# Kernel tuning notes

Measured on AMD Instinct MI355X. Metric: run time of the kernel, lower is better.

## Reference

```python
import jax, jax.numpy as jnp
import numpy as np

B = 131072
HIDDEN = [512, 512, 512, 512]
BETA = 20.0  # Softplus(beta=20)


def setup_inputs() -> dict:
    key = jax.random.key(0)
    dims = [3] + HIDDEN + [2]  # in_dim=3, out = div_mat_dim + 1 = 2
    n_layers = len(dims) - 1
    ks = jax.random.split(key, 1 + 2 * n_layers)
    d = {"tx": jax.random.normal(ks[0], (B, 3), dtype=jnp.float32)}
    for i, (din, dout) in enumerate(zip(dims[:-1], dims[1:])):
        lim = 1.0 / np.sqrt(din)  # torch nn.Linear default init
        d[f"W{i}"] = jax.random.uniform(ks[1 + 2 * i], (dout, din), jnp.float32, -lim, lim)
        d[f"b{i}"] = jax.random.uniform(ks[2 + 2 * i], (dout,), jnp.float32, -lim, lim)
    return d


def reference(tx, W0, b0, W1, b1, W2, b2, W3, b3, W4, b4):
    params = [(W0, b0), (W1, b1), (W2, b2), (W3, b3), (W4, b4)]

    def mlp(x):
        h = x
        for W, b in params[:-1]:
            # torch Softplus(beta=20): softplus(beta*x)/beta
            h = jax.nn.softplus(BETA * (h @ W.T + b)) / BETA
        W, b = params[-1]
        return h @ W.T + b  # [..., 2]: (stream fn s, pressure p)

    # div_A_matrix builds the 2x2 antisymmetric matrix A with A[0,1]=s, A[1,0]=-s.
    # vmap(jacrev(div_A_matrix)) then einsum('...ii') over the spatial cols (x,y)
    # reduces exactly to u = (ds/dy, -ds/dx). Per-sample grads of s are obtained
    # with one vectorized backward pass (samples are independent).
    g = jax.grad(lambda t: mlp(t)[:, 0].sum())(tx)  # [B, 3] cols = (t, x, y)
    u = jnp.stack([g[:, 2], -g[:, 1]], axis=1)      # [B, 2]
    p = mlp(tx)[:, -1:]                              # [B, 1]
    # torch .squeeze(0) is a no-op for B > 1
    return jnp.concatenate([u, p], axis=1)           # [B, 3]
```

## Files before the change

kernel.cpp:

```cpp
#include <hip/hip_runtime.h>

typedef _Float16 f16;
typedef __attribute__((ext_vector_type(8))) _Float16 f16x8;
typedef __attribute__((ext_vector_type(4))) float f32x4;

#define BT   131072
#define DD   512
#define TM   32
#define MEFF 96
#define NBLK (BT / TM)

__device__ __forceinline__ void stA(char* ab, int row, int colbyte, float v) {
    *(f16*)(ab + row * 1024 + (colbyte ^ ((row & 7) << 4))) = (f16)v;
}
__device__ __forceinline__ f16x8 ldA8(const char* ab, int row, int kbyte) {
    return *(const f16x8*)(ab + row * 1024 + (kbyte ^ ((row & 7) << 4)));
}

__device__ __forceinline__ f16x8 cvt8(const float* q) {
    float4 u0 = *(const float4*)q;
    float4 u1 = *(const float4*)(q + 4);
    f16x8 r;
    r[0] = (f16)u0.x; r[1] = (f16)u0.y; r[2] = (f16)u0.z; r[3] = (f16)u0.w;
    r[4] = (f16)u1.x; r[5] = (f16)u1.y; r[6] = (f16)u1.z; r[7] = (f16)u1.w;
    return r;
}

__global__ void prep_w(const float* __restrict__ W1, const float* __restrict__ W2,
                       const float* __restrict__ W3, f16* __restrict__ wp) {
    int tid = blockIdx.x * 256 + threadIdx.x;
    if (tid >= 3 * 16 * 32 * 64) return;
    int lane = tid & 63;
    int frag = tid >> 6;
    int nsub = frag & 31;
    int sk   = (frag >> 5) & 15;
    int l    = frag >> 9;
    const float* W = (l == 0) ? W1 : (l == 1) ? W2 : W3;
    int n = nsub * 16 + (lane & 15);
    int k = sk * 32 + (lane >> 4) * 8;
    ((f16x8*)wp)[tid] = cvt8(W + n * DD + k);
}

#define MFMA_SK(skc, Q0, Q1, Q2, Q3)                                           \
    _Pragma("unroll")                                                          \
    for (int m = 0; m < 6; ++m) {                                              \
        f16x8 a = ldA8(ab, m * 16 + l15, (skc) * 64 + g16 * 16);               \
        acc[m][0] = __builtin_amdgcn_mfma_f32_16x16x32_f16(a, Q0, acc[m][0], 0, 0, 0); \
        acc[m][1] = __builtin_amdgcn_mfma_f32_16x16x32_f16(a, Q1, acc[m][1], 0, 0, 0); \
        acc[m][2] = __builtin_amdgcn_mfma_f32_16x16x32_f16(a, Q2, acc[m][2], 0, 0, 0); \
        acc[m][3] = __builtin_amdgcn_mfma_f32_16x16x32_f16(a, Q3, acc[m][3], 0, 0, 0); \
    }

#define LOADB(Q0, Q1, Q2, Q3, skc)                                             \
    if constexpr (PREP) {                                                      \
        const f16x8* p = wB + (size_t)((skc) * 32) * 64;                       \
        Q0 = p[0]; Q1 = p[64]; Q2 = p[128]; Q3 = p[192];                       \
    } else {                                                                   \
        const float* q = Wl + (size_t)(wv * 64 + l15) * DD + (skc) * 32 + g16 * 8; \
        Q0 = cvt8(q);                                                          \
        Q1 = cvt8(q + 16 * DD);                                                \
        Q2 = cvt8(q + 32 * DD);                                                \
        Q3 = cvt8(q + 48 * DD);                                                \
    }

template<bool PREP>
__global__ __launch_bounds__(512) void mlp_fused(
    const float* __restrict__ tx,
    const float* __restrict__ W0, const float* __restrict__ b0v,
    const float* __restrict__ W1, const float* __restrict__ b1v,
    const float* __restrict__ W2, const float* __restrict__ b2v,
    const float* __restrict__ W3, const float* __restrict__ b3v,
    const float* __restrict__ W4, const float* __restrict__ b4v,
    const f16* __restrict__ wp, float* __restrict__ out)
{
    __shared__ __align__(16) short abuf_s[MEFF * DD];
    __shared__ float txb[TM * 3];
    char* ab = (char*)abuf_s;

    const int tid  = threadIdx.x;
    const int lane = tid & 63;
    const int wv   = tid >> 6;
    const int g16  = lane >> 4;
    const int l15  = lane & 15;
    const long s0  = (long)blockIdx.x * TM;

    if (tid < TM * 3) txb[tid] = tx[s0 * 3 + tid];
    __syncthreads();

    {
        int n = tid;
        float w0 = W0[n * 3 + 0], w1 = W0[n * 3 + 1], w2 = W0[n * 3 + 2], bb = b0v[n];
        #pragma unroll 4
        for (int s = 0; s < TM; ++s) {
            float z  = fmaf(w0, txb[s * 3], fmaf(w1, txb[s * 3 + 1], fmaf(w2, txb[s * 3 + 2], bb)));
            float aa = fabsf(z);
            float e  = __expf(-20.f * aa);
            float dd = 1.f + e;
            float h  = fmaxf(z, 0.f) + __logf(dd) * 0.05f;
            float sg = (z > 0.f ? 1.f : e) * __builtin_amdgcn_rcpf(dd);
            stA(ab, s,          n * 2, h);
            stA(ab, TM + s,     n * 2, sg * w1);
            stA(ab, 2 * TM + s, n * 2, sg * w2);
        }
    }
    __syncthreads();

    for (int l = 0; l < 3; ++l) {
        const float* Wl = (l == 0) ? W1 : (l == 1) ? W2 : W3;
        const float* bl = (l == 0) ? b1v : (l == 1) ? b2v : b3v;
        const f16x8* wB = (const f16x8*)wp + (size_t)l * (16 * 32 * 64)
                        + (size_t)(wv * 4) * 64 + lane;

        f32x4 acc[6][4];
        #pragma unroll
        for (int m = 0; m < 6; ++m)
            #pragma unroll
            for (int n = 0; n < 4; ++n)
                acc[m][n] = f32x4{0.f, 0.f, 0.f, 0.f};

        f16x8 B0, B1, B2, B3, C0, C1, C2, C3;
        LOADB(B0, B1, B2, B3, 0)
        #pragma unroll 2
        for (int sk = 0; sk < 16; sk += 2) {
            LOADB(C0, C1, C2, C3, sk + 1)
            MFMA_SK(sk, B0, B1, B2, B3)
            if (sk + 2 < 16) { LOADB(B0, B1, B2, B3, sk + 2) }
            MFMA_SK(sk + 1, C0, C1, C2, C3)
        }

        __syncthreads();

        #pragma unroll
        for (int m = 0; m < 2; ++m)
            #pragma unroll
            for (int n = 0; n < 4; ++n) {
                float bias = bl[wv * 64 + n * 16 + l15];
                int   cb   = (wv * 64 + n * 16 + l15) * 2;
                #pragma unroll
                for (int r = 0; r < 4; ++r) {
                    int row = m * 16 + g16 * 4 + r;
                    float z  = acc[m][n][r] + bias;
                    float aa = fabsf(z);
                    float e  = __expf(-20.f * aa);
                    float dd = 1.f + e;
                    float h  = fmaxf(z, 0.f) + __logf(dd) * 0.05f;
                    float sg = (z > 0.f ? 1.f : e) * __builtin_amdgcn_rcpf(dd);
                    stA(ab, row,      cb, h);
                    stA(ab, row + 32, cb, sg * acc[m + 2][n][r]);
                    stA(ab, row + 64, cb, sg * acc[m + 4][n][r]);
                }
            }
        __syncthreads();
    }

    {
        const int kb = lane * 8;
        float wsr[8], wpr[8];
        #pragma unroll
        for (int j = 0; j < 8; ++j) { wsr[j] = W4[kb + j]; wpr[j] = W4[DD + kb + j]; }
        float bp = b4v[1];
        #pragma unroll
        for (int i = 0; i < 4; ++i) {
            int s = wv * 4 + i;
            f16x8 hh = ldA8(ab, s,      lane * 16);
            f16x8 hx = ldA8(ab, 32 + s, lane * 16);
            f16x8 hy = ldA8(ab, 64 + s, lane * 16);
            float dy = 0.f, dx = 0.f, dp = 0.f;
            #pragma unroll
            for (int j = 0; j < 8; ++j) {
                dy = fmaf(wsr[j], (float)hy[j], dy);
                dx = fmaf(wsr[j], (float)hx[j], dx);
                dp = fmaf(wpr[j], (float)hh[j], dp);
            }
            #pragma unroll
            for (int mk = 1; mk < 64; mk <<= 1) {
                dy += __shfl_xor(dy, mk);
                dx += __shfl_xor(dx, mk);
                dp += __shfl_xor(dp, mk);
            }
            if (lane == 0) {
                float* o = out + (s0 + s) * 3;
                o[0] = dy;
                o[1] = -dx;
                o[2] = dp + bp;
            }
        }
    }
}

extern "C" void kernel_launch(void* const* d_in, const int* in_sizes, int n_in,
                              void* d_out, int out_size, void* d_ws, size_t ws_size,
                              hipStream_t stream) {
    const float* tx = (const float*)d_in[0];
    const float* W0 = (const float*)d_in[1]; const float* b0 = (const float*)d_in[2];
    const float* W1 = (const float*)d_in[3]; const float* b1 = (const float*)d_in[4];
    const float* W2 = (const float*)d_in[5]; const float* b2 = (const float*)d_in[6];
    const float* W3 = (const float*)d_in[7]; const float* b3 = (const float*)d_in[8];
    const float* W4 = (const float*)d_in[9]; const float* b4 = (const float*)d_in[10];
    float* out = (float*)d_out;

    const size_t need = (size_t)3 * 512 * 512 * sizeof(f16);
    if (ws_size >= need) {
        f16* wp = (f16*)d_ws;
        prep_w<<<(3 * 16 * 32 * 64 + 255) / 256, 256, 0, stream>>>(W1, W2, W3, wp);
        mlp_fused<true><<<NBLK, 512, 0, stream>>>(tx, W0, b0, W1, b1, W2, b2, W3, b3, W4, b4, wp, out);
    } else {
        mlp_fused<false><<<NBLK, 512, 0, stream>>>(tx, W0, b0, W1, b1, W2, b2, W3, b3, W4, b4, nullptr, out);
    }
}
```

Baseline: 758.8 us.

## Replace block barriers with per-chunk LDS flags so waves start on ready K-chunks

Replaces the __syncthreads barriers between layers with LDS flag counters. Each wave publishes readiness of the two K-chunks (64 columns) it writes, and starts its GEMM loop at its own chunk, rotating through the rest, so it can begin on freshly written data while other waves finish their epilogues. A progress counter stands in for the barrier that guards overwriting the activation buffer. This adds spin-wait overhead and loses the double-buffered B-fragment prefetch, since loads now sit right before each wait, and it relies on workgroup-scope atomics ordering the LDS stores.

```diff
diff --git a/kernel.cpp b/kernel.cpp
--- a/kernel.cpp
+++ b/kernel.cpp
@@ -24,6 +24,15 @@
     r[0] = (f16)u0.x; r[1] = (f16)u0.y; r[2] = (f16)u0.z; r[3] = (f16)u0.w;
     r[4] = (f16)u1.x; r[5] = (f16)u1.y; r[6] = (f16)u1.z; r[7] = (f16)u1.w;
     return r;
+}
+
+__device__ __forceinline__ void waitge(int* p, int v) {
+    if (__hip_atomic_load(p, __ATOMIC_ACQUIRE, __HIP_MEMORY_SCOPE_WORKGROUP) >= v) return;
+    while (__hip_atomic_load(p, __ATOMIC_ACQUIRE, __HIP_MEMORY_SCOPE_WORKGROUP) < v)
+        __builtin_amdgcn_s_sleep(1);
+}
+__device__ __forceinline__ void st_rel(int* p, int v) {
+    __hip_atomic_store(p, v, __ATOMIC_RELEASE, __HIP_MEMORY_SCOPE_WORKGROUP);
 }
 
 __global__ void prep_w(const float* __restrict__ W1, const float* __restrict__ W2,
@@ -41,22 +50,22 @@
     ((f16x8*)wp)[tid] = cvt8(W + n * DD + k);
 }
 
-#define MFMA_SK(skc, Q0, Q1, Q2, Q3)                                           \
+#define MFMA_SK(cc, Q0, Q1, Q2, Q3)                                            \
     _Pragma("unroll")                                                          \
     for (int m = 0; m < 6; ++m) {                                              \
-        f16x8 a = ldA8(ab, m * 16 + l15, (skc) * 64 + g16 * 16);               \
+        f16x8 a = ldA8(ab, m * 16 + l15, (cc) * 64 + g16 * 16);                \
         acc[m][0] = __builtin_amdgcn_mfma_f32_16x16x32_f16(a, Q0, acc[m][0], 0, 0, 0); \
         acc[m][1] = __builtin_amdgcn_mfma_f32_16x16x32_f16(a, Q1, acc[m][1], 0, 0, 0); \
         acc[m][2] = __builtin_amdgcn_mfma_f32_16x16x32_f16(a, Q2, acc[m][2], 0, 0, 0); \
         acc[m][3] = __builtin_amdgcn_mfma_f32_16x16x32_f16(a, Q3, acc[m][3], 0, 0, 0); \
     }
 
-#define LOADB(Q0, Q1, Q2, Q3, skc)                                             \
+#define LOADB(Q0, Q1, Q2, Q3, cc)                                              \
     if constexpr (PREP) {                                                      \
-        const f16x8* p = wB + (size_t)((skc) * 32) * 64;                       \
+        const f16x8* p = wB + ((size_t)(cc) << 11);                            \
         Q0 = p[0]; Q1 = p[64]; Q2 = p[128]; Q3 = p[192];                       \
     } else {                                                                   \
-        const float* q = Wl + (size_t)(wv * 64 + l15) * DD + (skc) * 32 + g16 * 8; \
+        const float* q = Wl + (size_t)(wv * 64 + l15) * DD + (cc) * 32 + g16 * 8; \
         Q0 = cvt8(q);                                                          \
         Q1 = cvt8(q + 16 * DD);                                                \
         Q2 = cvt8(q + 32 * DD);                                                \
@@ -75,6 +84,8 @@
 {
     __shared__ __align__(16) short abuf_s[MEFF * DD];
     __shared__ float txb[TM * 3];
+    __shared__ int ready[16];
+    __shared__ int progress[8];
     char* ab = (char*)abuf_s;
 
     const int tid  = threadIdx.x;
@@ -84,6 +95,8 @@
     const int l15  = lane & 15;
     const long s0  = (long)blockIdx.x * TM;
 
+    if (tid < 16) ready[tid] = 0;
+    if (tid >= 16 && tid < 24) progress[tid - 16] = 0;
     if (tid < TM * 3) txb[tid] = tx[s0 * 3 + tid];
     __syncthreads();
 
@@ -103,12 +116,12 @@
             stA(ab, 2 * TM + s, n * 2, sg * w2);
         }
     }
-    __syncthreads();
-
-    for (int l = 0; l < 3; ++l) {
-        const float* Wl = (l == 0) ? W1 : (l == 1) ? W2 : W3;
-        const float* bl = (l == 0) ? b1v : (l == 1) ? b2v : b3v;
-        const f16x8* wB = (const f16x8*)wp + (size_t)l * (16 * 32 * 64)
+    if (lane == 0) { st_rel(&ready[2 * wv], 1); st_rel(&ready[2 * wv + 1], 1); }
+
+    for (int li = 0; li < 3; ++li) {
+        const float* Wl = (li == 0) ? W1 : (li == 1) ? W2 : W3;
+        const float* bl = (li == 0) ? b1v : (li == 1) ? b2v : b3v;
+        const f16x8* wB = (const f16x8*)wp + (size_t)li * (16 * 32 * 64)
                         + (size_t)(wv * 4) * 64 + lane;
 
         f32x4 acc[6][4];
@@ -118,17 +131,19 @@
             for (int n = 0; n < 4; ++n)
                 acc[m][n] = f32x4{0.f, 0.f, 0.f, 0.f};
 
-        f16x8 B0, B1, B2, B3, C0, C1, C2, C3;
-        LOADB(B0, B1, B2, B3, 0)
+        int c = 2 * wv;
         #pragma unroll 2
-        for (int sk = 0; sk < 16; sk += 2) {
-            LOADB(C0, C1, C2, C3, sk + 1)
-            MFMA_SK(sk, B0, B1, B2, B3)
-            if (sk + 2 < 16) { LOADB(B0, B1, B2, B3, sk + 2) }
-            MFMA_SK(sk + 1, C0, C1, C2, C3)
+        for (int j = 0; j < 16; ++j) {
+            f16x8 b0, b1, b2, b3;
+            LOADB(b0, b1, b2, b3, c)
+            waitge(&ready[c], li + 1);
+            MFMA_SK(c, b0, b1, b2, b3)
+            c = (c + 1) & 15;
         }
-
-        __syncthreads();
+        if (lane == 0) st_rel(&progress[wv], li + 1);
+
+        #pragma unroll 1
+        for (int w = 0; w < 8; ++w) waitge(&progress[w], li + 1);
 
         #pragma unroll
         for (int m = 0; m < 2; ++m)
@@ -150,9 +165,11 @@
                     stA(ab, row + 64, cb, sg * acc[m + 4][n][r]);
                 }
             }
-        __syncthreads();
-    }
-
+        if (lane == 0) { st_rel(&ready[2 * wv], li + 2); st_rel(&ready[2 * wv + 1], li + 2); }
+    }
+
+    #pragma unroll 1
+    for (int cc = 0; cc < 16; ++cc) waitge(&ready[cc], 4);
     {
         const int kb = lane * 8;
         float wsr[8], wpr[8];
```

Measured after the change: 792.9 us. +4.5%, slower.
